# Kernel tuning notes

Measured on AMD Instinct MI355X. Metric: run time of the kernel, lower is better.

The kernel has to match this reference:

```python
import jax, jax.numpy as jnp
import numpy as np

N_BASIS = 8
CUTOFF = 5.0
NORM_FACTOR = 16.0


def setup_inputs() -> dict:
    key = jax.random.key(0)
    ks = jax.random.split(key, 10)
    N, E, C = 20000, 320000, 32
    s = 1.0 / np.sqrt(C)
    return {
        "node0": jax.random.normal(ks[0], (N, C), jnp.float32),
        "node1": jax.random.normal(ks[1], (N, C, 3), jnp.float32),
        "node2": jax.random.normal(ks[2], (N, C, 3, 3), jnp.float32),
        "rij": jax.random.normal(ks[3], (E, 3), jnp.float32) * 1.5,
        "Wrad": jax.random.normal(ks[4], (11, N_BASIS, C), jnp.float32) * 0.3,
        "U": jax.random.normal(ks[5], (3, C, C), jnp.float32) * s,
        "V": jax.random.normal(ks[6], (8, C, C), jnp.float32) * s,
        "Wg": jax.random.normal(ks[7], (3, C, C), jnp.float32) * s,
        "idx_i": jax.random.randint(ks[8], (E,), 0, N),
        "idx_j": jax.random.randint(ks[9], (E,), 0, N),
    }


def reference(node0, node1, node2, rij, Wrad, U, V, Wg, idx_i, idx_j):
    N, C = node0.shape
    # radial basis (Gaussian RBF * cosine cutoff envelope)
    dist = jnp.sqrt(jnp.sum(rij * rij, -1) + 1e-12)           # [E]
    rhat = rij / dist[:, None]                                 # [E,3]
    centers = jnp.linspace(0.5, CUTOFF, N_BASIS, dtype=node0.dtype)
    fc = 0.5 * (jnp.cos(jnp.pi * jnp.clip(dist / CUTOFF, 0.0, 1.0)) + 1.0)
    rbf = jnp.exp(-4.0 * (dist[:, None] - centers) ** 2) * fc[:, None]  # [E,B]
    # per-coupling-path radial filters: 11 paths (in_way, r_way, out_way)
    w = jnp.einsum('eb,pbc->pec', rbf, Wrad)                   # [11,E,C]
    # gather neighbor (node_j) features per edge
    g0 = node0[idx_j]                                          # [E,C]
    g1 = node1[idx_j]                                          # [E,C,3]
    g2 = node2[idx_j]                                          # [E,C,3,3]
    m1 = rhat                                                  # [E,3]
    m2 = rhat[:, :, None] * rhat[:, None, :]                   # [E,3,3]
    # graph conv: contract node_j tensor with r-way moment, weighted by radial filter
    # paths: 0:(0,0,0) 1:(0,1,1) 2:(0,2,2) 3:(1,0,1) 4:(1,1,0) 5:(1,1,2)
    #        6:(1,2,1) 7:(2,0,2) 8:(2,1,1) 9:(2,2,0) 10:(2,2,2)
    msg0 = (g0 * w[0]
            + jnp.einsum('eca,ea->ec', g1, m1) * w[4]
            + jnp.einsum('ecab,eab->ec', g2, m2) * w[9])
    msg1 = (jnp.einsum('ec,ea->eca', g0 * w[1], m1)
            + g1 * w[3][:, :, None]
            + jnp.einsum('eca,eab->ecb', g1, m2) * w[6][:, :, None]
            + jnp.einsum('ecab,eb->eca', g2, m1) * w[8][:, :, None])
    msg2 = (jnp.einsum('ec,eab->ecab', g0 * w[2], m2)
            + jnp.einsum('eca,eb->ecab', g1 * w[5][:, :, None], m1)
            + g2 * w[7][:, :, None, None]
            + jnp.einsum('ecab,ebd->ecad', g2, m2) * w[10][:, :, None, None])
    # scatter_add aggregation into per-atom features, normalized
    a0 = jax.ops.segment_sum(msg0, idx_i, num_segments=N) / NORM_FACTOR
    a1 = jax.ops.segment_sum(msg1, idx_i, num_segments=N) / NORM_FACTOR
    a2 = jax.ops.segment_sum(msg2, idx_i, num_segments=N) / NORM_FACTOR
    # multi-body self-interaction (2-body linear U + 3-body products V)
    y0 = (jnp.einsum('nc,cd->nd', a0, U[0])
          + jnp.einsum('nc,cd->nd', a0 * a0, V[0])
          + jnp.einsum('nc,cd->nd', jnp.einsum('nca,nca->nc', a1, a1), V[3])
          + jnp.einsum('nc,cd->nd', jnp.einsum('ncab,ncab->nc', a2, a2), V[6]))
    y1 = (jnp.einsum('nca,cd->nda', a1, U[1])
          + jnp.einsum('nca,cd->nda', a0[:, :, None] * a1, V[1])
          + jnp.einsum('nca,cd->nda', jnp.einsum('nca,ncab->ncb', a1, a2), V[5]))
    y2 = (jnp.einsum('ncab,cd->ndab', a2, U[2])
          + jnp.einsum('ncab,cd->ndab', a0[:, :, None, None] * a2, V[2])
          + jnp.einsum('ncab,cd->ndab', a1[:, :, :, None] * a1[:, :, None, :], V[4])
          + jnp.einsum('ncab,cd->ndab', jnp.einsum('ncab,ncbd->ncad', a2, a2), V[7]))
    # gated nonlinearity (scalar channel gates tensor ways) + residual add
    new0 = node0 + jax.nn.silu(y0 @ Wg[0])
    new1 = node1 + y1 * jax.nn.silu(y0 @ Wg[1])[:, :, None]
    new2 = node2 + y2 * jax.nn.silu(y0 @ Wg[2])[:, :, None, None]
    return (new0, new1, new2)
```

## Files before the change

kernel.cpp:

```cpp
#include <hip/hip_runtime.h>
#include <hip/hip_fp16.h>

#define NCH 32
#define NB 8
#define NPB 8

typedef __attribute__((ext_vector_type(2))) _Float16 half2r;

__device__ __forceinline__ unsigned short f2h(float f) {
    return __half_as_ushort(__float2half_rn(f));
}
__device__ __forceinline__ float h2f_lo(unsigned int u) {
    half2r v = __builtin_bit_cast(half2r, u);
    return (float)v.x;
}
__device__ __forceinline__ float h2f_hi(unsigned int u) {
    half2r v = __builtin_bit_cast(half2r, u);
    return (float)v.y;
}

__device__ __forceinline__ float fdot2u(unsigned int a, unsigned int b, float c) {
#if __has_builtin(__builtin_amdgcn_fdot2)
    return __builtin_amdgcn_fdot2(__builtin_bit_cast(half2r, a),
                                  __builtin_bit_cast(half2r, b), c, false);
#else
    half2r av = __builtin_bit_cast(half2r, a);
    half2r bv = __builtin_bit_cast(half2r, b);
    return c + (float)av.x * (float)bv.x + (float)av.y * (float)bv.y;
#endif
}

__device__ __forceinline__ void acc8h(float& y, uint4 w, uint4 f) {
    y = fdot2u(w.x, f.x, y);
    y = fdot2u(w.y, f.y, y);
    y = fdot2u(w.z, f.z, y);
    y = fdot2u(w.w, f.w, y);
}
__device__ __forceinline__ void acc8fh(float& y, uint4 w, float4 a, float4 b) {
    y += h2f_lo(w.x) * a.x + h2f_hi(w.x) * a.y + h2f_lo(w.y) * a.z + h2f_hi(w.y) * a.w
       + h2f_lo(w.z) * b.x + h2f_hi(w.z) * b.y + h2f_lo(w.w) * b.z + h2f_hi(w.w) * b.w;
}

__global__ __launch_bounds__(256) void wprep_kernel(
    const float* __restrict__ U, const float* __restrict__ V,
    const float* __restrict__ Wg, unsigned short* __restrict__ wswz)
{
    int idx = blockIdx.x * 256 + threadIdx.x;
    if (idx >= 14 * 1024) return;
    int m = idx >> 10, r = idx & 1023;
    int c = r >> 5, d = r & 31;
    float v;
    if (m < 3)       v = U[m * 1024 + c * 32 + d];
    else if (m < 11) v = V[(m - 3) * 1024 + c * 32 + d];
    else             v = Wg[(m - 11) * 1024 + c * 32 + d];
    wswz[m * 1024 + (c >> 3) * 256 + d * 8 + (c & 7)] = f2h(v);
}

__global__ __launch_bounds__(256) void wprep_rad_kernel(
    const float* __restrict__ Wrad, unsigned int* __restrict__ wradp)
{
    int idx = blockIdx.x * 256 + threadIdx.x;
    if (idx >= 11 * 4 * 32) return;
    int c = idx & 31, bb = (idx >> 5) & 3, p = idx >> 7;
    float lo = Wrad[p * 256 + (2 * bb) * 32 + c] * (1.0f / 16.0f);
    float hi = Wrad[p * 256 + (2 * bb + 1) * 32 + c] * (1.0f / 16.0f);
    wradp[(p * 4 + bb) * 32 + c] = (unsigned int)f2h(lo) | ((unsigned int)f2h(hi) << 16);
}

__global__ __launch_bounds__(256) void hist_kernel(
    const int* __restrict__ idx_i, int* __restrict__ counts, int E)
{
    int e = blockIdx.x * 256 + threadIdx.x;
    if (e < E) atomicAdd(&counts[idx_i[e]], 1);
}

__global__ __launch_bounds__(256) void scan_reduce_kernel(
    const int* __restrict__ counts, int* __restrict__ blocksums, int N)
{
    const int tid = threadIdx.x;
    const int base = blockIdx.x * 1024;
    int v = 0;
    #pragma unroll
    for (int k = 0; k < 4; ++k) {
        int i = base + tid * 4 + k;
        if (i < N) v += counts[i];
    }
    #pragma unroll
    for (int off = 1; off < 64; off <<= 1) v += __shfl_xor(v, off, 64);
    __shared__ int wsum[4];
    if ((tid & 63) == 0) wsum[tid >> 6] = v;
    __syncthreads();
    if (tid == 0) blocksums[blockIdx.x] = wsum[0] + wsum[1] + wsum[2] + wsum[3];
}

__global__ void scan_top_kernel(
    const int* __restrict__ blocksums, int* __restrict__ bases,
    int* __restrict__ offsets, int nb, int N)
{
    int l = threadIdx.x;
    int v = (l < nb) ? blocksums[l] : 0;
    int incl = v;
    #pragma unroll
    for (int off = 1; off < 64; off <<= 1) {
        int t = __shfl_up(incl, off, 64);
        if (l >= off) incl += t;
    }
    if (l < nb) bases[l] = incl - v;
    if (l == nb - 1) offsets[N] = incl;
}

__global__ __launch_bounds__(256) void scan_write_kernel(
    int* __restrict__ cursor, const int* __restrict__ bases,
    int* __restrict__ offsets, int N)
{
    const int tid = threadIdx.x;
    const int i0 = blockIdx.x * 1024 + tid * 4;
    int v[4]; int lsum = 0;
    #pragma unroll
    for (int k = 0; k < 4; ++k) {
        int i = i0 + k;
        v[k] = (i < N) ? cursor[i] : 0;
        lsum += v[k];
    }
    int incl = lsum;
    #pragma unroll
    for (int off = 1; off < 64; off <<= 1) {
        int t = __shfl_up(incl, off, 64);
        if ((tid & 63) >= off) incl += t;
    }
    __shared__ int wsum[4];
    if ((tid & 63) == 63) wsum[tid >> 6] = incl;
    __syncthreads();
    int add = bases[blockIdx.x];
    for (int w = 0; w < (tid >> 6); ++w) add += wsum[w];
    int run = add + incl - lsum;
    #pragma unroll
    for (int k = 0; k < 4; ++k) {
        int i = i0 + k;
        if (i < N) { offsets[i] = run; cursor[i] = run; run += v[k]; }
    }
}

__global__ __launch_bounds__(256) void scatter_meta_kernel(
    const int* __restrict__ idx_i, const int* __restrict__ idx_j,
    const float* __restrict__ rij, int* __restrict__ cursor,
    int* __restrict__ jord, float4* __restrict__ meta2, int E)
{
    int e = blockIdx.x * 256 + threadIdx.x;
    if (e >= E) return;
    float rx = rij[3 * e + 0], ry = rij[3 * e + 1], rz = rij[3 * e + 2];
    float dist = sqrtf(rx * rx + ry * ry + rz * rz + 1e-12f);
    float inv = 1.0f / dist;
    float tcl = fminf(dist * 0.2f, 1.0f);
    float fc = 0.5f * (cosf(3.14159265358979f * tcl) + 1.0f);
    float rbf[NB];
    #pragma unroll
    for (int b = 0; b < NB; ++b) {
        float dd = dist - (0.5f + (float)b * (4.5f / 7.0f));
        rbf[b] = expf(-4.0f * dd * dd) * fc;
    }
    unsigned int rb01 = (unsigned int)f2h(rbf[0]) | ((unsigned int)f2h(rbf[1]) << 16);
    unsigned int rb23 = (unsigned int)f2h(rbf[2]) | ((unsigned int)f2h(rbf[3]) << 16);
    unsigned int rb45 = (unsigned int)f2h(rbf[4]) | ((unsigned int)f2h(rbf[5]) << 16);
    unsigned int rb67 = (unsigned int)f2h(rbf[6]) | ((unsigned int)f2h(rbf[7]) << 16);
    int slot = atomicAdd(&cursor[idx_i[e]], 1);
    jord[slot] = idx_j[e];
    meta2[2 * slot + 0] = make_float4(rx * inv, ry * inv, rz * inv, __uint_as_float(rb01));
    meta2[2 * slot + 1] = make_float4(__uint_as_float(rb23), __uint_as_float(rb45),
                                      __uint_as_float(rb67), 0.0f);
}

__global__ __launch_bounds__(256) void transpose_nodes_kernel(
    const float* __restrict__ node0, const float* __restrict__ node1,
    const float* __restrict__ node2, unsigned short* __restrict__ n0h,
    unsigned short* __restrict__ n1h, unsigned short* __restrict__ n2h, int N)
{
    int n = blockIdx.x * 8 + (threadIdx.x >> 5);
    int c = threadIdx.x & 31;
    if (n >= N) return;
    n0h[n * 32 + c] = f2h(node0[n * 32 + c]);
    #pragma unroll
    for (int a = 0; a < 3; ++a) n1h[n * 96 + a * 32 + c] = f2h(node1[n * 96 + c * 3 + a]);
    #pragma unroll
    for (int k = 0; k < 9; ++k) n2h[n * 288 + k * 32 + c] = f2h(node2[n * 288 + c * 9 + k]);
}

__global__ __launch_bounds__(256) void aggregate_kernel(
    const unsigned short* __restrict__ n0h, const unsigned short* __restrict__ n1h,
    const unsigned short* __restrict__ n2h, const unsigned int* __restrict__ wradp,
    const int* __restrict__ jord, const float4* __restrict__ meta2,
    const int* __restrict__ offsets,
    float* __restrict__ a0, float* __restrict__ a1, float* __restrict__ a2,
    int N)
{
    const int c = threadIdx.x & 31;
    const int g = threadIdx.x >> 5;
    const int n = blockIdx.x * NPB + g;
    if (n >= N) return;

    unsigned int wr[11][4];
    #pragma unroll
    for (int p = 0; p < 11; ++p)
        #pragma unroll
        for (int bb = 0; bb < 4; ++bb)
            wr[p][bb] = wradp[(p * 4 + bb) * 32 + c];

    const int beg = offsets[n], end = offsets[n + 1];

    float A0 = 0.f;
    float A1[3] = {0.f, 0.f, 0.f};
    float A2[9] = {0.f, 0.f, 0.f, 0.f, 0.f, 0.f, 0.f, 0.f, 0.f};

    float4 M0n = make_float4(0.f, 0.f, 0.f, 0.f), M1n = M0n;
    unsigned short G0n = 0, G1n[3] = {0, 0, 0}, G2n[9] = {};

    int s = beg;
    if (s < end) {
        int j = jord[s];
        M0n = meta2[2 * s + 0]; M1n = meta2[2 * s + 1];
        G0n = n0h[j * 32 + c];
        #pragma unroll
        for (int a = 0; a < 3; ++a) G1n[a] = n1h[j * 96 + a * 32 + c];
        #pragma unroll
        for (int k = 0; k < 9; ++k) G2n[k] = n2h[j * 288 + k * 32 + c];
    }

    while (s < end) {
        float4 M0 = M0n, M1 = M1n;
        float G0 = __half2float(__ushort_as_half(G0n));
        float G1[3], G2[9];
        #pragma unroll
        for (int a = 0; a < 3; ++a) G1[a] = __half2float(__ushort_as_half(G1n[a]));
        #pragma unroll
        for (int k = 0; k < 9; ++k) G2[k] = __half2float(__ushort_as_half(G2n[k]));

        int sn = s + 1;
        if (sn < end) {
            int j = jord[sn];
            M0n = meta2[2 * sn + 0]; M1n = meta2[2 * sn + 1];
            G0n = n0h[j * 32 + c];
            #pragma unroll
            for (int a = 0; a < 3; ++a) G1n[a] = n1h[j * 96 + a * 32 + c];
            #pragma unroll
            for (int k = 0; k < 9; ++k) G2n[k] = n2h[j * 288 + k * 32 + c];
        }

        float h[3] = { M0.x, M0.y, M0.z };
        unsigned int rb01 = __float_as_uint(M0.w);
        unsigned int rb23 = __float_as_uint(M1.x);
        unsigned int rb45 = __float_as_uint(M1.y);
        unsigned int rb67 = __float_as_uint(M1.z);

        float w[11];
        #pragma unroll
        for (int p = 0; p < 11; ++p)
            w[p] = fdot2u(rb01, wr[p][0],
                   fdot2u(rb23, wr[p][1],
                   fdot2u(rb45, wr[p][2],
                   fdot2u(rb67, wr[p][3], 0.0f))));

        float s1 = G1[0] * h[0] + G1[1] * h[1] + G1[2] * h[2];
        float tt[3];
        #pragma unroll
        for (int a = 0; a < 3; ++a)
            tt[a] = G2[a * 3 + 0] * h[0] + G2[a * 3 + 1] * h[1] + G2[a * 3 + 2] * h[2];
        float s2 = tt[0] * h[0] + tt[1] * h[1] + tt[2] * h[2];

        A0 += G0 * w[0] + s1 * w[4] + s2 * w[9];
        #pragma unroll
        for (int a = 0; a < 3; ++a)
            A1[a] += (G0 * w[1] + s1 * w[6]) * h[a] + G1[a] * w[3] + tt[a] * w[8];
        #pragma unroll
        for (int a = 0; a < 3; ++a) {
            float pre = G0 * w[2] * h[a] + G1[a] * w[5] + tt[a] * w[10];
            #pragma unroll
            for (int b = 0; b < 3; ++b)
                A2[a * 3 + b] += pre * h[b] + G2[a * 3 + b] * w[7];
        }
        s = sn;
    }

    a0[n * 32 + c] = A0;
    #pragma unroll
    for (int a = 0; a < 3; ++a) a1[n * 96 + a * 32 + c] = A1[a];
    #pragma unroll
    for (int k = 0; k < 9; ++k) a2[n * 288 + k * 32 + c] = A2[k];
}

__global__ __launch_bounds__(256) void node_kernel(
    const float* __restrict__ node0, const float* __restrict__ node1,
    const float* __restrict__ node2, const unsigned short* __restrict__ wswz,
    float* __restrict__ out0, float* __restrict__ out1, float* __restrict__ out2,
    int N)
{
    __shared__ alignas(16) unsigned short wT[14 * 1024];
    __shared__ alignas(16) unsigned short feat[NPB * 49 * 32];
    __shared__ alignas(16) float y0s[NPB][32];

    {
        const uint4* src = reinterpret_cast<const uint4*>(wswz);
        uint4* dst = reinterpret_cast<uint4*>(wT);
        for (int i = threadIdx.x; i < 14 * 128; i += 256) dst[i] = src[i];
    }

    const int g = threadIdx.x >> 5;
    const int lane = threadIdx.x & 31;
    const int n = blockIdx.x * NPB + g;
    const bool active = (n < N);

    if (active) {
        const int c = lane;
        float A0 = out0[n * 32 + c];
        float A1[3], A2[9];
        #pragma unroll
        for (int a = 0; a < 3; ++a) A1[a] = out1[n * 96 + a * 32 + c];
        #pragma unroll
        for (int k = 0; k < 9; ++k) A2[k] = out2[n * 288 + k * 32 + c];

        unsigned short* F = &feat[g * 49 * 32];
        F[0 * 32 + c] = f2h(A0);
        F[1 * 32 + c] = f2h(A0 * A0);
        F[2 * 32 + c] = f2h(A1[0] * A1[0] + A1[1] * A1[1] + A1[2] * A1[2]);
        float n2 = 0.f;
        #pragma unroll
        for (int k = 0; k < 9; ++k) n2 += A2[k] * A2[k];
        F[3 * 32 + c] = f2h(n2);
        #pragma unroll
        for (int a = 0; a < 3; ++a) {
            F[(4 + a) * 32 + c] = f2h(A1[a]);
            F[(7 + a) * 32 + c] = f2h(A0 * A1[a]);
        }
        #pragma unroll
        for (int b = 0; b < 3; ++b) {
            float s = A1[0] * A2[0 * 3 + b] + A1[1] * A2[1 * 3 + b] + A1[2] * A2[2 * 3 + b];
            F[(10 + b) * 32 + c] = f2h(s);
        }
        #pragma unroll
        for (int k = 0; k < 9; ++k) {
            F[(13 + k) * 32 + c] = f2h(A2[k]);
            F[(22 + k) * 32 + c] = f2h(A0 * A2[k]);
        }
        #pragma unroll
        for (int a = 0; a < 3; ++a)
            #pragma unroll
            for (int b = 0; b < 3; ++b)
                F[(31 + a * 3 + b) * 32 + c] = f2h(A1[a] * A1[b]);
        #pragma unroll
        for (int a = 0; a < 3; ++a)
            #pragma unroll
            for (int dd = 0; dd < 3; ++dd) {
                float s = A2[a * 3 + 0] * A2[0 * 3 + dd] + A2[a * 3 + 1] * A2[1 * 3 + dd]
                        + A2[a * 3 + 2] * A2[2 * 3 + dd];
                F[(40 + a * 3 + dd) * 32 + c] = f2h(s);
            }
    }
    __syncthreads();

    const int d = lane;
    float y0v = 0.f;
    float y1v[3] = {0.f, 0.f, 0.f};
    float y2v[9] = {0.f, 0.f, 0.f, 0.f, 0.f, 0.f, 0.f, 0.f, 0.f};

    if (active) {
        const uint4* W4 = reinterpret_cast<const uint4*>(wT);
        const uint4* F4 = reinterpret_cast<const uint4*>(&feat[g * 49 * 32]);
        for (int q = 0; q < 4; ++q) {
            const int q32d = q * 32 + d;
            acc8h(y0v, W4[0 * 128 + q32d], F4[0 * 4 + q]);
            acc8h(y0v, W4[3 * 128 + q32d], F4[1 * 4 + q]);
            acc8h(y0v, W4[6 * 128 + q32d], F4[2 * 4 + q]);
            acc8h(y0v, W4[9 * 128 + q32d], F4[3 * 4 + q]);
            uint4 wU1 = W4[1 * 128 + q32d];
            uint4 wV1 = W4[4 * 128 + q32d];
            uint4 wV5 = W4[8 * 128 + q32d];
            #pragma unroll
            for (int a = 0; a < 3; ++a) {
                acc8h(y1v[a], wU1, F4[(4 + a) * 4 + q]);
                acc8h(y1v[a], wV1, F4[(7 + a) * 4 + q]);
                acc8h(y1v[a], wV5, F4[(10 + a) * 4 + q]);
            }
            uint4 wU2 = W4[2 * 128 + q32d];
            uint4 wV2 = W4[5 * 128 + q32d];
            uint4 wV4 = W4[7 * 128 + q32d];
            uint4 wV7 = W4[10 * 128 + q32d];
            #pragma unroll
            for (int k = 0; k < 9; ++k) {
                acc8h(y2v[k], wU2, F4[(13 + k) * 4 + q]);
                acc8h(y2v[k], wV2, F4[(22 + k) * 4 + q]);
                acc8h(y2v[k], wV4, F4[(31 + k) * 4 + q]);
                acc8h(y2v[k], wV7, F4[(40 + k) * 4 + q]);
            }
        }
        y0s[g][d] = y0v;
    }
    __syncthreads();

    if (!active) return;

    float t0 = 0.f, t1 = 0.f, t2 = 0.f;
    {
        const uint4* W4 = reinterpret_cast<const uint4*>(wT);
        const float4* Y4 = reinterpret_cast<const float4*>(y0s[g]);
        #pragma unroll
        for (int q = 0; q < 4; ++q) {
            const int q32d = q * 32 + d;
            float4 ya = Y4[2 * q], yb = Y4[2 * q + 1];
            acc8fh(t0, W4[11 * 128 + q32d], ya, yb);
            acc8fh(t1, W4[12 * 128 + q32d], ya, yb);
            acc8fh(t2, W4[13 * 128 + q32d], ya, yb);
        }
    }
    float s0 = t0 / (1.0f + expf(-t0));
    float s1 = t1 / (1.0f + expf(-t1));
    float s2 = t2 / (1.0f + expf(-t2));

    out0[n * 32 + d] = node0[n * 32 + d] + s0;
    #pragma unroll
    for (int a = 0; a < 3; ++a)
        out1[n * 96 + d * 3 + a] = node1[n * 96 + d * 3 + a] + y1v[a] * s1;
    #pragma unroll
    for (int k = 0; k < 9; ++k)
        out2[n * 288 + d * 9 + k] = node2[n * 288 + d * 9 + k] + y2v[k] * s2;
}

extern "C" void kernel_launch(void* const* d_in, const int* in_sizes, int n_in,
                              void* d_out, int out_size, void* d_ws, size_t ws_size,
                              hipStream_t stream)
{
    const float* node0 = (const float*)d_in[0];
    const float* node1 = (const float*)d_in[1];
    const float* node2 = (const float*)d_in[2];
    const float* rij   = (const float*)d_in[3];
    const float* Wrad  = (const float*)d_in[4];
    const float* U     = (const float*)d_in[5];
    const float* V     = (const float*)d_in[6];
    const float* Wg    = (const float*)d_in[7];
    const int* idx_i   = (const int*)d_in[8];
    const int* idx_j   = (const int*)d_in[9];

    const int N = in_sizes[0] / 32;
    const int E = in_sizes[3] / 3;

    float* out0 = (float*)d_out;
    float* out1 = out0 + (size_t)N * 32;
    float* out2 = out1 + (size_t)N * 96;

    size_t off = 0;
    auto walloc = [&](size_t bytes) -> void* {
        off = (off + 63) & ~(size_t)63;
        void* p = (char*)d_ws + off;
        off += bytes;
        return p;
    };
    int*    cursor    = (int*)   walloc((size_t)N * 4);
    int*    offsets   = (int*)   walloc((size_t)(N + 1) * 4);
    int*    blocksums = (int*)   walloc(64 * 4);
    int*    bases     = (int*)   walloc(64 * 4);
    int*    jord      = (int*)   walloc((size_t)E * 4);
    float4* meta2     = (float4*)walloc((size_t)E * 2 * sizeof(float4));
    unsigned short* n0h = (unsigned short*)walloc((size_t)N * 32 * 2);
    unsigned short* n1h = (unsigned short*)walloc((size_t)N * 96 * 2);
    unsigned short* n2h = (unsigned short*)walloc((size_t)N * 288 * 2);
    unsigned short* wswz = (unsigned short*)walloc(14 * 1024 * 2);
    unsigned int*  wradp = (unsigned int*)walloc(11 * 4 * 32 * 4);
    (void)ws_size;

    const int nb = (N + 1023) / 1024;

    hipMemsetAsync(cursor, 0, (size_t)N * sizeof(int), stream);

    wprep_kernel<<<dim3(56), dim3(256), 0, stream>>>(U, V, Wg, wswz);
    wprep_rad_kernel<<<dim3(6), dim3(256), 0, stream>>>(Wrad, wradp);
    hist_kernel<<<dim3((E + 255) / 256), dim3(256), 0, stream>>>(idx_i, cursor, E);
    scan_reduce_kernel<<<dim3(nb), dim3(256), 0, stream>>>(cursor, blocksums, N);
    scan_top_kernel<<<dim3(1), dim3(64), 0, stream>>>(blocksums, bases, offsets, nb, N);
    scan_write_kernel<<<dim3(nb), dim3(256), 0, stream>>>(cursor, bases, offsets, N);
    scatter_meta_kernel<<<dim3((E + 255) / 256), dim3(256), 0, stream>>>(
        idx_i, idx_j, rij, cursor, jord, meta2, E);
    transpose_nodes_kernel<<<dim3((N + 7) / 8), dim3(256), 0, stream>>>(
        node0, node1, node2, n0h, n1h, n2h, N);

    aggregate_kernel<<<dim3((N + NPB - 1) / NPB), dim3(256), 0, stream>>>(
        n0h, n1h, n2h, wradp, jord, meta2, offsets, out0, out1, out2, N);

    node_kernel<<<dim3((N + NPB - 1) / NPB), dim3(256), 0, stream>>>(
        node0, node1, node2, wswz, out0, out1, out2, N);
}
```

Baseline: 286.4 us.

## Pack node features per channel into 32-byte records and split edges across wave halves

Node features are stored as an interleaved fp16 record per (node, channel), two uint4 per channel, so each gathered edge needs two 16-byte loads instead of thirteen 2-byte loads. The aggregate kernel now assigns a full 64-lane wave per node, with each half handling alternate edges, and combines the halves with an xor shuffle at the end. A deeper prefetch of jord indices is added. This cuts gather instruction count and raises memory-level parallelism per node, in exchange for half as many nodes per block, some padding bytes, and idle lanes when a node has an odd edge count.

```diff
diff --git a/kernel.cpp b/kernel.cpp
--- a/kernel.cpp
+++ b/kernel.cpp
@@ -17,6 +17,9 @@
 __device__ __forceinline__ float h2f_hi(unsigned int u) {
     half2r v = __builtin_bit_cast(half2r, u);
     return (float)v.y;
+}
+__device__ __forceinline__ unsigned int pack2h(float lo, float hi) {
+    return (unsigned int)f2h(lo) | ((unsigned int)f2h(hi) << 16);
 }
 
 __device__ __forceinline__ float fdot2u(unsigned int a, unsigned int b, float c) {
@@ -64,7 +67,7 @@
     int c = idx & 31, bb = (idx >> 5) & 3, p = idx >> 7;
     float lo = Wrad[p * 256 + (2 * bb) * 32 + c] * (1.0f / 16.0f);
     float hi = Wrad[p * 256 + (2 * bb + 1) * 32 + c] * (1.0f / 16.0f);
-    wradp[(p * 4 + bb) * 32 + c] = (unsigned int)f2h(lo) | ((unsigned int)f2h(hi) << 16);
+    wradp[(p * 4 + bb) * 32 + c] = pack2h(lo, hi);
 }
 
 __global__ __launch_bounds__(256) void hist_kernel(
@@ -159,10 +162,10 @@
         float dd = dist - (0.5f + (float)b * (4.5f / 7.0f));
         rbf[b] = expf(-4.0f * dd * dd) * fc;
     }
-    unsigned int rb01 = (unsigned int)f2h(rbf[0]) | ((unsigned int)f2h(rbf[1]) << 16);
-    unsigned int rb23 = (unsigned int)f2h(rbf[2]) | ((unsigned int)f2h(rbf[3]) << 16);
-    unsigned int rb45 = (unsigned int)f2h(rbf[4]) | ((unsigned int)f2h(rbf[5]) << 16);
-    unsigned int rb67 = (unsigned int)f2h(rbf[6]) | ((unsigned int)f2h(rbf[7]) << 16);
+    unsigned int rb01 = pack2h(rbf[0], rbf[1]);
+    unsigned int rb23 = pack2h(rbf[2], rbf[3]);
+    unsigned int rb45 = pack2h(rbf[4], rbf[5]);
+    unsigned int rb67 = pack2h(rbf[6], rbf[7]);
     int slot = atomicAdd(&cursor[idx_i[e]], 1);
     jord[slot] = idx_j[e];
     meta2[2 * slot + 0] = make_float4(rx * inv, ry * inv, rz * inv, __uint_as_float(rb01));
@@ -172,30 +175,42 @@
 
 __global__ __launch_bounds__(256) void transpose_nodes_kernel(
     const float* __restrict__ node0, const float* __restrict__ node1,
-    const float* __restrict__ node2, unsigned short* __restrict__ n0h,
-    unsigned short* __restrict__ n1h, unsigned short* __restrict__ n2h, int N)
+    const float* __restrict__ node2, uint4* __restrict__ ncomb, int N)
 {
     int n = blockIdx.x * 8 + (threadIdx.x >> 5);
     int c = threadIdx.x & 31;
     if (n >= N) return;
-    n0h[n * 32 + c] = f2h(node0[n * 32 + c]);
-    #pragma unroll
-    for (int a = 0; a < 3; ++a) n1h[n * 96 + a * 32 + c] = f2h(node1[n * 96 + c * 3 + a]);
-    #pragma unroll
-    for (int k = 0; k < 9; ++k) n2h[n * 288 + k * 32 + c] = f2h(node2[n * 288 + c * 9 + k]);
+    float G0 = node0[n * 32 + c];
+    float G1[3];
+    #pragma unroll
+    for (int a = 0; a < 3; ++a) G1[a] = node1[n * 96 + c * 3 + a];
+    float G2[9];
+    #pragma unroll
+    for (int k = 0; k < 9; ++k) G2[k] = node2[n * 288 + c * 9 + k];
+    uint4 P0, P1;
+    P0.x = pack2h(G0,    G1[0]);
+    P0.y = pack2h(G1[1], G1[2]);
+    P0.z = pack2h(G2[0], G2[1]);
+    P0.w = pack2h(G2[2], G2[3]);
+    P1.x = pack2h(G2[4], G2[5]);
+    P1.y = pack2h(G2[6], G2[7]);
+    P1.z = pack2h(G2[8], 0.0f);
+    P1.w = 0u;
+    ncomb[(size_t)n * 64 + c]      = P0;
+    ncomb[(size_t)n * 64 + 32 + c] = P1;
 }
 
 __global__ __launch_bounds__(256) void aggregate_kernel(
-    const unsigned short* __restrict__ n0h, const unsigned short* __restrict__ n1h,
-    const unsigned short* __restrict__ n2h, const unsigned int* __restrict__ wradp,
+    const uint4* __restrict__ ncomb, const unsigned int* __restrict__ wradp,
     const int* __restrict__ jord, const float4* __restrict__ meta2,
     const int* __restrict__ offsets,
     float* __restrict__ a0, float* __restrict__ a1, float* __restrict__ a2,
     int N)
 {
-    const int c = threadIdx.x & 31;
-    const int g = threadIdx.x >> 5;
-    const int n = blockIdx.x * NPB + g;
+    const int lane = threadIdx.x & 63;
+    const int c = lane & 31;
+    const int side = lane >> 5;
+    const int n = blockIdx.x * 4 + (threadIdx.x >> 6);
     if (n >= N) return;
 
     unsigned int wr[11][4];
@@ -206,85 +221,109 @@
             wr[p][bb] = wradp[(p * 4 + bb) * 32 + c];
 
     const int beg = offsets[n], end = offsets[n + 1];
+    const int nit = (end - beg + 1) >> 1;
 
     float A0 = 0.f;
     float A1[3] = {0.f, 0.f, 0.f};
     float A2[9] = {0.f, 0.f, 0.f, 0.f, 0.f, 0.f, 0.f, 0.f, 0.f};
 
+    int e = beg + side;
+    bool vn = (e < end);
+    int jn = 0;
+    if (vn) jn = jord[e];
+    bool vn2 = (e + 2 < end);
+    int jn2 = 0;
+    if (vn2) jn2 = jord[e + 2];
+
+    uint4 P0n = {0, 0, 0, 0}, P1n = {0, 0, 0, 0};
     float4 M0n = make_float4(0.f, 0.f, 0.f, 0.f), M1n = M0n;
-    unsigned short G0n = 0, G1n[3] = {0, 0, 0}, G2n[9] = {};
-
-    int s = beg;
-    if (s < end) {
-        int j = jord[s];
-        M0n = meta2[2 * s + 0]; M1n = meta2[2 * s + 1];
-        G0n = n0h[j * 32 + c];
-        #pragma unroll
-        for (int a = 0; a < 3; ++a) G1n[a] = n1h[j * 96 + a * 32 + c];
-        #pragma unroll
-        for (int k = 0; k < 9; ++k) G2n[k] = n2h[j * 288 + k * 32 + c];
-    }
-
-    while (s < end) {
-        float4 M0 = M0n, M1 = M1n;
-        float G0 = __half2float(__ushort_as_half(G0n));
-        float G1[3], G2[9];
-        #pragma unroll
-        for (int a = 0; a < 3; ++a) G1[a] = __half2float(__ushort_as_half(G1n[a]));
-        #pragma unroll
-        for (int k = 0; k < 9; ++k) G2[k] = __half2float(__ushort_as_half(G2n[k]));
-
-        int sn = s + 1;
-        if (sn < end) {
-            int j = jord[sn];
-            M0n = meta2[2 * sn + 0]; M1n = meta2[2 * sn + 1];
-            G0n = n0h[j * 32 + c];
-            #pragma unroll
-            for (int a = 0; a < 3; ++a) G1n[a] = n1h[j * 96 + a * 32 + c];
-            #pragma unroll
-            for (int k = 0; k < 9; ++k) G2n[k] = n2h[j * 288 + k * 32 + c];
-        }
-
-        float h[3] = { M0.x, M0.y, M0.z };
-        unsigned int rb01 = __float_as_uint(M0.w);
-        unsigned int rb23 = __float_as_uint(M1.x);
-        unsigned int rb45 = __float_as_uint(M1.y);
-        unsigned int rb67 = __float_as_uint(M1.z);
-
-        float w[11];
-        #pragma unroll
-        for (int p = 0; p < 11; ++p)
-            w[p] = fdot2u(rb01, wr[p][0],
-                   fdot2u(rb23, wr[p][1],
-                   fdot2u(rb45, wr[p][2],
-                   fdot2u(rb67, wr[p][3], 0.0f))));
-
-        float s1 = G1[0] * h[0] + G1[1] * h[1] + G1[2] * h[2];
-        float tt[3];
-        #pragma unroll
-        for (int a = 0; a < 3; ++a)
-            tt[a] = G2[a * 3 + 0] * h[0] + G2[a * 3 + 1] * h[1] + G2[a * 3 + 2] * h[2];
-        float s2 = tt[0] * h[0] + tt[1] * h[1] + tt[2] * h[2];
-
-        A0 += G0 * w[0] + s1 * w[4] + s2 * w[9];
-        #pragma unroll
-        for (int a = 0; a < 3; ++a)
-            A1[a] += (G0 * w[1] + s1 * w[6]) * h[a] + G1[a] * w[3] + tt[a] * w[8];
-        #pragma unroll
-        for (int a = 0; a < 3; ++a) {
-            float pre = G0 * w[2] * h[a] + G1[a] * w[5] + tt[a] * w[10];
-            #pragma unroll
-            for (int b = 0; b < 3; ++b)
-                A2[a * 3 + b] += pre * h[b] + G2[a * 3 + b] * w[7];
-        }
-        s = sn;
-    }
-
-    a0[n * 32 + c] = A0;
-    #pragma unroll
-    for (int a = 0; a < 3; ++a) a1[n * 96 + a * 32 + c] = A1[a];
-    #pragma unroll
-    for (int k = 0; k < 9; ++k) a2[n * 288 + k * 32 + c] = A2[k];
+    if (vn) {
+        const uint4* src = ncomb + ((size_t)jn << 6) + c;
+        P0n = src[0];
+        P1n = src[32];
+        M0n = meta2[2 * e + 0];
+        M1n = meta2[2 * e + 1];
+    }
+
+    for (int it = 0; it < nit; ++it) {
+        const uint4 P0 = P0n, P1 = P1n;
+        const float4 M0 = M0n, M1 = M1n;
+        const bool v = vn;
+
+        const int en = e + 2;
+        vn = vn2;
+        jn = jn2;
+        if (vn) {
+            const uint4* src = ncomb + ((size_t)jn << 6) + c;
+            P0n = src[0];
+            P1n = src[32];
+            M0n = meta2[2 * en + 0];
+            M1n = meta2[2 * en + 1];
+        }
+        vn2 = (en + 2 < end);
+        if (vn2) jn2 = jord[en + 2];
+        e = en;
+
+        if (v) {
+            const float h0 = M0.x, h1 = M0.y, h2 = M0.z;
+            const unsigned int rb01 = __float_as_uint(M0.w);
+            const unsigned int rb23 = __float_as_uint(M1.x);
+            const unsigned int rb45 = __float_as_uint(M1.y);
+            const unsigned int rb67 = __float_as_uint(M1.z);
+
+            float w[11];
+            #pragma unroll
+            for (int p = 0; p < 11; ++p)
+                w[p] = fdot2u(rb01, wr[p][0],
+                       fdot2u(rb23, wr[p][1],
+                       fdot2u(rb45, wr[p][2],
+                       fdot2u(rb67, wr[p][3], 0.0f))));
+
+            const float G0   = h2f_lo(P0.x);
+            float G1[3];
+            G1[0] = h2f_hi(P0.x); G1[1] = h2f_lo(P0.y); G1[2] = h2f_hi(P0.y);
+            float G2[9];
+            G2[0] = h2f_lo(P0.z); G2[1] = h2f_hi(P0.z);
+            G2[2] = h2f_lo(P0.w); G2[3] = h2f_hi(P0.w);
+            G2[4] = h2f_lo(P1.x); G2[5] = h2f_hi(P1.x);
+            G2[6] = h2f_lo(P1.y); G2[7] = h2f_hi(P1.y);
+            G2[8] = h2f_lo(P1.z);
+
+            const float hh[3] = {h0, h1, h2};
+            const float s1 = G1[0] * h0 + G1[1] * h1 + G1[2] * h2;
+            float tt[3];
+            #pragma unroll
+            for (int a = 0; a < 3; ++a)
+                tt[a] = G2[a * 3 + 0] * h0 + G2[a * 3 + 1] * h1 + G2[a * 3 + 2] * h2;
+            const float s2 = tt[0] * h0 + tt[1] * h1 + tt[2] * h2;
+
+            A0 += G0 * w[0] + s1 * w[4] + s2 * w[9];
+            #pragma unroll
+            for (int a = 0; a < 3; ++a)
+                A1[a] += (G0 * w[1] + s1 * w[6]) * hh[a] + G1[a] * w[3] + tt[a] * w[8];
+            #pragma unroll
+            for (int a = 0; a < 3; ++a) {
+                float pre = G0 * w[2] * hh[a] + G1[a] * w[5] + tt[a] * w[10];
+                #pragma unroll
+                for (int b = 0; b < 3; ++b)
+                    A2[a * 3 + b] += pre * hh[b] + G2[a * 3 + b] * w[7];
+            }
+        }
+    }
+
+    A0 += __shfl_xor(A0, 32, 64);
+    #pragma unroll
+    for (int a = 0; a < 3; ++a) A1[a] += __shfl_xor(A1[a], 32, 64);
+    #pragma unroll
+    for (int k = 0; k < 9; ++k) A2[k] += __shfl_xor(A2[k], 32, 64);
+
+    if (side == 0) {
+        a0[n * 32 + c] = A0;
+        #pragma unroll
+        for (int a = 0; a < 3; ++a) a1[n * 96 + a * 32 + c] = A1[a];
+        #pragma unroll
+        for (int k = 0; k < 9; ++k) a2[n * 288 + k * 32 + c] = A2[k];
+    }
 }
 
 __global__ __launch_bounds__(256) void node_kernel(
@@ -458,9 +497,7 @@
     int*    bases     = (int*)   walloc(64 * 4);
     int*    jord      = (int*)   walloc((size_t)E * 4);
     float4* meta2     = (float4*)walloc((size_t)E * 2 * sizeof(float4));
-    unsigned short* n0h = (unsigned short*)walloc((size_t)N * 32 * 2);
-    unsigned short* n1h = (unsigned short*)walloc((size_t)N * 96 * 2);
-    unsigned short* n2h = (unsigned short*)walloc((size_t)N * 288 * 2);
+    uint4*  ncomb     = (uint4*) walloc((size_t)N * 64 * sizeof(uint4));
     unsigned short* wswz = (unsigned short*)walloc(14 * 1024 * 2);
     unsigned int*  wradp = (unsigned int*)walloc(11 * 4 * 32 * 4);
     (void)ws_size;
@@ -478,10 +515,10 @@
     scatter_meta_kernel<<<dim3((E + 255) / 256), dim3(256), 0, stream>>>(
         idx_i, idx_j, rij, cursor, jord, meta2, E);
     transpose_nodes_kernel<<<dim3((N + 7) / 8), dim3(256), 0, stream>>>(
-        node0, node1, node2, n0h, n1h, n2h, N);
-
-    aggregate_kernel<<<dim3((N + NPB - 1) / NPB), dim3(256), 0, stream>>>(
-        n0h, n1h, n2h, wradp, jord, meta2, offsets, out0, out1, out2, N);
+        node0, node1, node2, ncomb, N);
+
+    aggregate_kernel<<<dim3((N + 3) / 4), dim3(256), 0, stream>>>(
+        ncomb, wradp, jord, meta2, offsets, out0, out1, out2, N);
 
     node_kernel<<<dim3((N + NPB - 1) / NPB), dim3(256), 0, stream>>>(
         node0, node1, node2, wswz, out0, out1, out2, N);
```

Result: faster. 274.6 us (-4.1%).
